# Performance work log

Measured on AMD Instinct MI355X. Metric: run time of the kernel, lower is better.

Reference implementation:

```python
import jax, jax.numpy as jnp
import numpy as np
from jax import lax

TEMPERATURE = 30.0
BN_EPS = 1e-5


def setup_inputs() -> dict:
    key = jax.random.key(0)
    ks = jax.random.split(key, 9)
    B, H, W, C_in = 32, 64, 64, 128
    n_filters, r_filters, n_kernels = 128, 4, 4
    x = jax.random.normal(ks[0], (B, H, W, C_in), dtype=jnp.float32)
    reduction_kernel = jax.random.normal(ks[1], (C_in, r_filters), dtype=jnp.float32) * 0.02
    attention_kernel = jax.random.normal(ks[2], (r_filters, n_kernels), dtype=jnp.float32) * 0.02
    conv_kernels = jax.random.normal(ks[3], (n_kernels, 3, 3, C_in, n_filters), dtype=jnp.float32) * 0.05
    bias = jax.random.normal(ks[4], (n_kernels, n_filters), dtype=jnp.float32) * 0.05
    bn_scale = jax.random.uniform(ks[5], (n_filters,), dtype=jnp.float32, minval=0.5, maxval=1.5)
    bn_bias = jax.random.normal(ks[6], (n_filters,), dtype=jnp.float32) * 0.1
    bn_mean = jax.random.normal(ks[7], (n_filters,), dtype=jnp.float32) * 0.1
    bn_var = jax.random.uniform(ks[8], (n_filters,), dtype=jnp.float32, minval=0.5, maxval=1.5)
    return {"x": x, "reduction_kernel": reduction_kernel, "attention_kernel": attention_kernel,
            "conv_kernels": conv_kernels, "bias": bias, "bn_scale": bn_scale, "bn_bias": bn_bias,
            "bn_mean": bn_mean, "bn_var": bn_var}


def reference(x, reduction_kernel, attention_kernel, conv_kernels, bias, bn_scale, bn_bias, bn_mean, bn_var):
    # x: [B,H,W,C_in] NHWC. Inference mode (training=False): BN uses running stats.
    B = x.shape[0]
    # Squeeze-style routing: global average pool -> reduce -> relu -> attention over experts.
    pool = jnp.mean(x, axis=(1, 2))                             # [B, C_in]
    pool_red = jax.nn.relu(pool @ reduction_kernel)             # [B, r]
    attention = jax.nn.softmax((pool_red @ attention_kernel) / TEMPERATURE, axis=-1)  # [B, K]
    # Soft mixture of conv expert kernels, per sample.
    w_mixed = jnp.einsum('bk,khwio->bhwio', attention, conv_kernels)  # [B,kH,kW,C_in,F]

    def per_sample_conv(xi, wi):
        # xi: [H,W,C_in], wi: [kH,kW,C_in,F]
        return lax.conv_general_dilated(xi[None], wi, window_strides=(1, 1), padding='SAME',
                                        dimension_numbers=('NHWC', 'HWIO', 'NHWC'))[0]

    y = jax.vmap(per_sample_conv)(x, w_mixed)                   # [B,H,W,F]
    b_mixed = attention @ bias                                  # [B, F]
    y = y + b_mixed[:, None, None, :]
    # BatchNorm (inference) + relu
    inv = bn_scale * lax.rsqrt(bn_var + BN_EPS)
    y = (y - bn_mean) * inv + bn_bias
    return jax.nn.relu(y)
```

## Files before the change

kernel.cpp:

```cpp
#include <hip/hip_runtime.h>

typedef short bf16x8 __attribute__((ext_vector_type(8)));
typedef float f32x4 __attribute__((ext_vector_type(4)));
typedef unsigned int u32x4 __attribute__((ext_vector_type(4)));
typedef unsigned short u16x4 __attribute__((ext_vector_type(4)));

__device__ __forceinline__ unsigned short f2bf(float f) {
  unsigned u = __builtin_bit_cast(unsigned, f);
  u = (u + 0x7FFFu + ((u >> 16) & 1u)) >> 16;
  return (unsigned short)u;
}

__global__ __launch_bounds__(256) void k_pool_cvt(const float* __restrict__ x,
                                                  unsigned short* __restrict__ xb,
                                                  float* __restrict__ pp) {
  const int slice = blockIdx.x;
  const int b = blockIdx.y;
  const int t = threadIdx.x;
  const int c4 = (t & 31) * 4;
  const int seg = t >> 5;
  const size_t base = ((size_t)b * 4096 + slice * 256 + seg * 32) * 128;
  const float* xp = x + base;
  unsigned short* xbp = xb + base;
  f32x4 s = {0.f, 0.f, 0.f, 0.f};
  for (int p = 0; p < 32; ++p) {
    f32x4 v = *(const f32x4*)(xp + p * 128 + c4);
    s += v;
    u16x4 h;
    h.x = f2bf(v.x); h.y = f2bf(v.y); h.z = f2bf(v.z); h.w = f2bf(v.w);
    *(u16x4*)(xbp + p * 128 + c4) = h;
  }
  __shared__ f32x4 red[256];
  red[t] = s;
  __syncthreads();
  if (t < 32) {
    f32x4 tot = red[t];
#pragma unroll
    for (int g = 1; g < 8; ++g) tot += red[g * 32 + t];
    *(f32x4*)(pp + (size_t)(b * 16 + slice) * 128 + t * 4) = tot;
  }
}

__global__ __launch_bounds__(128) void k_route(const float* __restrict__ pp,
    const float* __restrict__ redk, const float* __restrict__ attk,
    const float* __restrict__ bias, const float* __restrict__ bns,
    const float* __restrict__ bnb, const float* __restrict__ bnm,
    const float* __restrict__ bnv,
    float* __restrict__ att_ws, float* __restrict__ beta_ws,
    float* __restrict__ alpha_ws) {
  const int b = blockIdx.x, t = threadIdx.x;
  __shared__ float pool[128];
  __shared__ float att[4];
  {
    float s = 0.f;
    for (int i = 0; i < 16; ++i) s += pp[(size_t)(b * 16 + i) * 128 + t];
    pool[t] = s * (1.f / 4096.f);
  }
  __syncthreads();
  if (t == 0) {
    float pr[4];
    for (int r = 0; r < 4; ++r) {
      float s = 0.f;
      for (int c = 0; c < 128; ++c) s += pool[c] * redk[c * 4 + r];
      pr[r] = fmaxf(s, 0.f);
    }
    float lgt[4]; float mx = -1e30f;
    for (int k = 0; k < 4; ++k) {
      float s = 0.f;
      for (int r = 0; r < 4; ++r) s += pr[r] * attk[r * 4 + k];
      lgt[k] = s * (1.f / 30.f);
      mx = fmaxf(mx, lgt[k]);
    }
    float den = 0.f;
    for (int k = 0; k < 4; ++k) { lgt[k] = expf(lgt[k] - mx); den += lgt[k]; }
    for (int k = 0; k < 4; ++k) { att[k] = lgt[k] / den; att_ws[b * 4 + k] = att[k]; }
  }
  __syncthreads();
  {
    float bm = 0.f;
    for (int k = 0; k < 4; ++k) bm += att[k] * bias[k * 128 + t];
    const float inv = bns[t] * rsqrtf(bnv[t] + 1e-5f);
    beta_ws[b * 128 + t] = (bm - bnm[t]) * inv + bnb[t];
    alpha_ws[t] = inv;
  }
}

__global__ __launch_bounds__(256) void k_mixw(const float* __restrict__ ck,
                                              const float* __restrict__ att_ws,
                                              unsigned short* __restrict__ w_ws) {
  const int tap = blockIdx.x;
  const int b = blockIdx.y;
  const int t = threadIdx.x;
  const float a0 = att_ws[b * 4 + 0], a1 = att_ws[b * 4 + 1];
  const float a2 = att_ws[b * 4 + 2], a3 = att_ws[b * 4 + 3];
  const float* ckp = ck + (size_t)tap * 16384;
  __shared__ unsigned short lds_t[128 * 136];
#pragma unroll 4
  for (int it = 0; it < 16; ++it) {
    const int i4 = t + it * 256;
    const int idx = i4 * 4;
    const int c = idx >> 7, f = idx & 127;
    f32x4 v0 = *(const f32x4*)(ckp + idx);
    f32x4 v1 = *(const f32x4*)(ckp + idx + 147456);
    f32x4 v2 = *(const f32x4*)(ckp + idx + 2 * 147456);
    f32x4 v3 = *(const f32x4*)(ckp + idx + 3 * 147456);
#pragma unroll
    for (int e = 0; e < 4; ++e)
      lds_t[(f + e) * 136 + c] = f2bf(a0 * v0[e] + a1 * v1[e] + a2 * v2[e] + a3 * v3[e]);
  }
  __syncthreads();
#pragma unroll
  for (int it = 0; it < 8; ++it) {
    const int m = t + it * 256;
    const int f = m >> 4, oo = m & 15;
    const int h = oo >> 3, o = oo & 7;
    unsigned short* dst = w_ws + ((size_t)b * 18 + h * 9 + tap) * 8192
                        + (size_t)(f * 8 + (o ^ (f & 7))) * 8;
    *(bf16x8*)dst = *(const bf16x8*)(lds_t + f * 136 + oo * 8);
  }
}

__device__ __forceinline__ void stage_w16(char* dst, const unsigned short* src, int t) {
#pragma unroll
  for (int j = 0; j < 4; ++j) {
    const int i = t + j * 256;
    __builtin_amdgcn_global_load_lds(
        (const __attribute__((address_space(1))) void*)(src + (size_t)i * 8),
        (__attribute__((address_space(3))) void*)(dst + i * 16), 16, 0, 0);
  }
}

__device__ __forceinline__ void stage_x_half(char* xt, const unsigned short* xbp,
                                             int r0, int h, int t) {
#pragma unroll
  for (int j = 0; j < 12; ++j) {
    const int i = t + j * 256;
    const int jr = i >> 9;
    const int pix = (i & 511) >> 3;
    const int oct = i & 7;
    const int soct = oct ^ (pix & 7);
    const int rr = r0 - 1 + jr;
    char* dst = xt + i * 16;
    if ((unsigned)rr < 64u) {
      __builtin_amdgcn_global_load_lds(
          (const __attribute__((address_space(1))) void*)
              (xbp + ((size_t)(rr * 64 + pix)) * 128 + h * 64 + soct * 8),
          (__attribute__((address_space(3))) void*)dst, 16, 0, 0);
    } else {
      *(u32x4*)dst = (u32x4){0, 0, 0, 0};
    }
  }
}

__global__ __launch_bounds__(256, 2) void k_conv(const unsigned short* __restrict__ xb,
                                                 const unsigned short* __restrict__ w_ws,
                                                 const float* __restrict__ alpha_ws,
                                                 const float* __restrict__ beta_ws,
                                                 float* __restrict__ out) {
  extern __shared__ char lds[];
  char* xt = lds;
  char* wlds = lds + 49152;

  const int orig = blockIdx.x;
  const int wg = (orig & 7) * 64 + (orig >> 3);
  const int b = wg >> 4;
  const int tile = wg & 15;
  const int t = threadIdx.x;
  const int lane = t & 63, wm = t >> 6;
  const int lr = lane & 15, lg = lane >> 4;
  const int r0 = tile * 4;

  const unsigned short* xbp = xb + (size_t)b * 4096 * 128;
  const unsigned short* wsrc = w_ws + (size_t)b * 18 * 8192;

  f32x4 acc[4][8] = {};
  const bf16x8 zero = {};

  int abase[3][4];
  bool aval[3][4];
#pragma unroll
  for (int d = 0; d < 3; ++d)
#pragma unroll
    for (int mf = 0; mf < 4; ++mf) {
      const int col = mf * 16 + lr + d - 1;
      const bool v = (unsigned)col < 64u;
      aval[d][mf] = v;
      abase[d][mf] = v ? ((col * 128 + lg * 16) ^ ((col & 7) << 4)) : 0;
    }
  int bbase[8];
#pragma unroll
  for (int nf = 0; nf < 8; ++nf) {
    const int f = nf * 16 + lr;
    bbase[nf] = (f * 128 + lg * 16) ^ ((f & 7) << 4);
  }

  stage_x_half(xt, xbp, r0, 0, t);
  stage_w16(wlds, wsrc, t);
  asm volatile("s_waitcnt vmcnt(0) lgkmcnt(0)" ::: "memory");
  __builtin_amdgcn_s_barrier();
  asm volatile("" ::: "memory");

#pragma unroll
  for (int s = 0; s < 18; ++s) {
    const int tap = s % 9;
    char* cb = wlds + ((s & 1) << 14);
    if (s == 9) stage_x_half(xt, xbp, r0, 1, t);
    if (s < 17) stage_w16(wlds + (((s + 1) & 1) << 14),
                          wsrc + (size_t)(s + 1) * 8192, t);
    if (s == 9)       asm volatile("s_waitcnt vmcnt(4) lgkmcnt(0)" ::: "memory");
    else if (s < 17)  asm volatile("s_waitcnt vmcnt(4)" ::: "memory");
    else              asm volatile("s_waitcnt vmcnt(0)" ::: "memory");
    __builtin_amdgcn_s_barrier();
    asm volatile("" ::: "memory");

    const int d = tap % 3;
    const int jrow = wm + tap / 3;
#pragma unroll
    for (int kc = 0; kc < 2; ++kc) {
      const int kx = kc << 6;
      bf16x8 afr[4], bfr[8];
#pragma unroll
      for (int mf = 0; mf < 4; ++mf) {
        bf16x8 v = *(const bf16x8*)(xt + ((abase[d][mf] ^ kx) + jrow * 8192));
        afr[mf] = aval[d][mf] ? v : zero;
      }
#pragma unroll
      for (int nf = 0; nf < 8; ++nf)
        bfr[nf] = *(const bf16x8*)(cb + (bbase[nf] ^ kx));
      __builtin_amdgcn_s_setprio(1);
#pragma unroll
      for (int mf = 0; mf < 4; ++mf)
#pragma unroll
        for (int nf = 0; nf < 8; ++nf)
          acc[mf][nf] = __builtin_amdgcn_mfma_f32_16x16x32_bf16(afr[mf], bfr[nf],
                                                                acc[mf][nf], 0, 0, 0);
      __builtin_amdgcn_s_setprio(0);
    }
    asm volatile("" ::: "memory");
    __builtin_amdgcn_s_barrier();
  }

  float af[8], bt[8];
#pragma unroll
  for (int nf = 0; nf < 8; ++nf) {
    const int f = nf * 16 + lr;
    af[nf] = alpha_ws[f];
    bt[nf] = beta_ws[b * 128 + f];
  }
  float* op = out + (size_t)b * 4096 * 128;
  const int row = r0 + wm;
#pragma unroll
  for (int mf = 0; mf < 4; ++mf) {
#pragma unroll
    for (int r = 0; r < 4; ++r) {
      const int col = mf * 16 + lg * 4 + r;
#pragma unroll
      for (int nf = 0; nf < 8; ++nf) {
        const int f = nf * 16 + lr;
        const float v = acc[mf][nf][r] * af[nf] + bt[nf];
        op[(size_t)(row * 64 + col) * 128 + f] = fmaxf(v, 0.f);
      }
    }
  }
}

extern "C" void kernel_launch(void* const* d_in, const int* in_sizes, int n_in,
                              void* d_out, int out_size, void* d_ws, size_t ws_size,
                              hipStream_t stream) {
  const float* x    = (const float*)d_in[0];
  const float* redk = (const float*)d_in[1];
  const float* attk = (const float*)d_in[2];
  const float* ck   = (const float*)d_in[3];
  const float* bias = (const float*)d_in[4];
  const float* bns  = (const float*)d_in[5];
  const float* bnbb = (const float*)d_in[6];
  const float* bnm  = (const float*)d_in[7];
  const float* bnv  = (const float*)d_in[8];
  float* out = (float*)d_out;

  char* ws = (char*)d_ws;
  unsigned short* xb   = (unsigned short*)ws;
  unsigned short* w_ws = (unsigned short*)(ws + 33554432);
  float* pp       = (float*)(ws + 42991616);
  float* att_ws   = (float*)(ws + 43253760);
  float* beta_ws  = (float*)(ws + 43254272);
  float* alpha_ws = (float*)(ws + 43270656);

  k_pool_cvt<<<dim3(16, 32), 256, 0, stream>>>(x, xb, pp);
  k_route<<<32, 128, 0, stream>>>(pp, redk, attk, bias, bns, bnbb, bnm, bnv,
                                  att_ws, beta_ws, alpha_ws);
  k_mixw<<<dim3(9, 32), 256, 0, stream>>>(ck, att_ws, w_ws);
  k_conv<<<512, 256, 81920, stream>>>(xb, w_ws, alpha_ws, beta_ws, out);
}
```

Before: 89.35 us.

## Double conv row tile per workgroup and restructure mixed-weight kernel across batches

The conv kernel now computes 8 output rows per workgroup instead of 4. Each wave handles two rows, so every weight fragment loaded from LDS feeds twice as many MFMAs, and the grid halves to 256 blocks with larger LDS and one block per CU. The weight-mixing kernel is reorganised so each block loads one tap/channel/filter sub-tile of the expert kernels once and writes mixed bf16 weights for all 32 samples. This avoids re-reading the expert kernels for every sample. The cost is fewer resident waves per CU, more accumulator registers, and a non-unrolled stage loop that computes column offsets at run time.

```diff
diff --git a/kernel.cpp b/kernel.cpp
--- a/kernel.cpp
+++ b/kernel.cpp
@@ -88,35 +88,47 @@
 __global__ __launch_bounds__(256) void k_mixw(const float* __restrict__ ck,
                                               const float* __restrict__ att_ws,
                                               unsigned short* __restrict__ w_ws) {
-  const int tap = blockIdx.x;
-  const int b = blockIdx.y;
+  const int bx = blockIdx.x;
+  const int tap = bx >> 4;
+  const int cq = (bx >> 2) & 3;
+  const int fq = bx & 3;
   const int t = threadIdx.x;
-  const float a0 = att_ws[b * 4 + 0], a1 = att_ws[b * 4 + 1];
-  const float a2 = att_ws[b * 4 + 2], a3 = att_ws[b * 4 + 3];
-  const float* ckp = ck + (size_t)tap * 16384;
-  __shared__ unsigned short lds_t[128 * 136];
-#pragma unroll 4
-  for (int it = 0; it < 16; ++it) {
-    const int i4 = t + it * 256;
-    const int idx = i4 * 4;
-    const int c = idx >> 7, f = idx & 127;
-    f32x4 v0 = *(const f32x4*)(ckp + idx);
-    f32x4 v1 = *(const f32x4*)(ckp + idx + 147456);
-    f32x4 v2 = *(const f32x4*)(ckp + idx + 2 * 147456);
-    f32x4 v3 = *(const f32x4*)(ckp + idx + 3 * 147456);
-#pragma unroll
-    for (int e = 0; e < 4; ++e)
-      lds_t[(f + e) * 136 + c] = f2bf(a0 * v0[e] + a1 * v1[e] + a2 * v2[e] + a3 * v3[e]);
+  __shared__ float cw[4][32][32];
+  __shared__ float attl[128];
+  if (t < 128) attl[t] = att_ws[t];
+  {
+    const int k = t >> 6, c = (t & 63) >> 1, f0 = (t & 1) * 16;
+    const float* src = ck + ((size_t)(k * 9 + tap) * 128 + cq * 32 + c) * 128
+                          + fq * 32 + f0;
+    *(f32x4*)&cw[k][c][f0]      = *(const f32x4*)(src);
+    *(f32x4*)&cw[k][c][f0 + 4]  = *(const f32x4*)(src + 4);
+    *(f32x4*)&cw[k][c][f0 + 8]  = *(const f32x4*)(src + 8);
+    *(f32x4*)&cw[k][c][f0 + 12] = *(const f32x4*)(src + 12);
   }
   __syncthreads();
-#pragma unroll
-  for (int it = 0; it < 8; ++it) {
-    const int m = t + it * 256;
-    const int f = m >> 4, oo = m & 15;
-    const int h = oo >> 3, o = oo & 7;
-    unsigned short* dst = w_ws + ((size_t)b * 18 + h * 9 + tap) * 8192
-                        + (size_t)(f * 8 + (o ^ (f & 7))) * 8;
-    *(bf16x8*)dst = *(const bf16x8*)(lds_t + f * 136 + oo * 8);
+  const int f = t & 31, o = (t >> 5) & 3, sh = t >> 7;
+  const int fp = fq * 32 + f;
+  const int h = cq >> 1;
+  const int oslab = (cq & 1) * 4 + o;
+  const int chunk = fp * 8 + (oslab ^ (fp & 7));
+  float wv[4][8];
+#pragma unroll
+  for (int k = 0; k < 4; ++k)
+#pragma unroll
+    for (int j = 0; j < 8; ++j) wv[k][j] = cw[k][o * 8 + j][f];
+#pragma unroll
+  for (int bs = 0; bs < 16; ++bs) {
+    const int b = sh * 16 + bs;
+    const float a0 = attl[b * 4 + 0], a1 = attl[b * 4 + 1];
+    const float a2 = attl[b * 4 + 2], a3 = attl[b * 4 + 3];
+    bf16x8 ov;
+#pragma unroll
+    for (int j = 0; j < 8; ++j) {
+      const float v = a0 * wv[0][j] + a1 * wv[1][j] + a2 * wv[2][j] + a3 * wv[3][j];
+      ov[j] = (short)f2bf(v);
+    }
+    *(bf16x8*)(w_ws + (size_t)b * 147456 + (size_t)(h * 9 + tap) * 8192
+               + (size_t)chunk * 8) = ov;
   }
 }
 
@@ -133,7 +145,7 @@
 __device__ __forceinline__ void stage_x_half(char* xt, const unsigned short* xbp,
                                              int r0, int h, int t) {
 #pragma unroll
-  for (int j = 0; j < 12; ++j) {
+  for (int j = 0; j < 20; ++j) {
     const int i = t + j * 256;
     const int jr = i >> 9;
     const int pix = (i & 511) >> 3;
@@ -152,41 +164,30 @@
   }
 }
 
-__global__ __launch_bounds__(256, 2) void k_conv(const unsigned short* __restrict__ xb,
+__global__ __launch_bounds__(256, 1) void k_conv(const unsigned short* __restrict__ xb,
                                                  const unsigned short* __restrict__ w_ws,
                                                  const float* __restrict__ alpha_ws,
                                                  const float* __restrict__ beta_ws,
                                                  float* __restrict__ out) {
   extern __shared__ char lds[];
   char* xt = lds;
-  char* wlds = lds + 49152;
+  char* wlds = lds + 81920;
 
   const int orig = blockIdx.x;
-  const int wg = (orig & 7) * 64 + (orig >> 3);
-  const int b = wg >> 4;
-  const int tile = wg & 15;
+  const int wg = (orig & 7) * 32 + (orig >> 3);
+  const int b = wg >> 3;
+  const int tile = wg & 7;
   const int t = threadIdx.x;
   const int lane = t & 63, wm = t >> 6;
   const int lr = lane & 15, lg = lane >> 4;
-  const int r0 = tile * 4;
+  const int r0 = tile * 8;
 
   const unsigned short* xbp = xb + (size_t)b * 4096 * 128;
   const unsigned short* wsrc = w_ws + (size_t)b * 18 * 8192;
 
-  f32x4 acc[4][8] = {};
+  f32x4 acc[8][8] = {};
   const bf16x8 zero = {};
 
-  int abase[3][4];
-  bool aval[3][4];
-#pragma unroll
-  for (int d = 0; d < 3; ++d)
-#pragma unroll
-    for (int mf = 0; mf < 4; ++mf) {
-      const int col = mf * 16 + lr + d - 1;
-      const bool v = (unsigned)col < 64u;
-      aval[d][mf] = v;
-      abase[d][mf] = v ? ((col * 128 + lg * 16) ^ ((col & 7) << 4)) : 0;
-    }
   int bbase[8];
 #pragma unroll
   for (int nf = 0; nf < 8; ++nf) {
@@ -200,9 +201,10 @@
   __builtin_amdgcn_s_barrier();
   asm volatile("" ::: "memory");
 
-#pragma unroll
   for (int s = 0; s < 18; ++s) {
-    const int tap = s % 9;
+    const int tap = (s >= 9) ? s - 9 : s;
+    const int dr = (tap * 11) >> 5;
+    const int dw = tap - dr * 3;
     char* cb = wlds + ((s & 1) << 14);
     if (s == 9) stage_x_half(xt, xbp, r0, 1, t);
     if (s < 17) stage_w16(wlds + (((s + 1) & 1) << 14),
@@ -213,27 +215,39 @@
     __builtin_amdgcn_s_barrier();
     asm volatile("" ::: "memory");
 
-    const int d = tap % 3;
-    const int jrow = wm + tap / 3;
+    int cA[4]; bool vA[4];
+#pragma unroll
+    for (int cf = 0; cf < 4; ++cf) {
+      const int col = cf * 16 + lr + dw - 1;
+      vA[cf] = (unsigned)col < 64u;
+      const int cc = col & 63;
+      cA[cf] = (cc * 128 + lg * 16) ^ ((cc & 7) << 4);
+    }
+    const int ro0 = (2 * wm + dr) * 8192;
+
 #pragma unroll
     for (int kc = 0; kc < 2; ++kc) {
       const int kx = kc << 6;
-      bf16x8 afr[4], bfr[8];
-#pragma unroll
-      for (int mf = 0; mf < 4; ++mf) {
-        bf16x8 v = *(const bf16x8*)(xt + ((abase[d][mf] ^ kx) + jrow * 8192));
-        afr[mf] = aval[d][mf] ? v : zero;
-      }
+      bf16x8 afr[2][4], bfr[8];
+#pragma unroll
+      for (int rh = 0; rh < 2; ++rh)
+#pragma unroll
+        for (int cf = 0; cf < 4; ++cf) {
+          bf16x8 v = *(const bf16x8*)(xt + (ro0 + rh * 8192 + (cA[cf] ^ kx)));
+          afr[rh][cf] = vA[cf] ? v : zero;
+        }
 #pragma unroll
       for (int nf = 0; nf < 8; ++nf)
         bfr[nf] = *(const bf16x8*)(cb + (bbase[nf] ^ kx));
       __builtin_amdgcn_s_setprio(1);
 #pragma unroll
-      for (int mf = 0; mf < 4; ++mf)
-#pragma unroll
-        for (int nf = 0; nf < 8; ++nf)
-          acc[mf][nf] = __builtin_amdgcn_mfma_f32_16x16x32_bf16(afr[mf], bfr[nf],
-                                                                acc[mf][nf], 0, 0, 0);
+      for (int rh = 0; rh < 2; ++rh)
+#pragma unroll
+        for (int cf = 0; cf < 4; ++cf)
+#pragma unroll
+          for (int nf = 0; nf < 8; ++nf)
+            acc[rh * 4 + cf][nf] = __builtin_amdgcn_mfma_f32_16x16x32_bf16(
+                afr[rh][cf], bfr[nf], acc[rh * 4 + cf][nf], 0, 0, 0);
       __builtin_amdgcn_s_setprio(0);
     }
     asm volatile("" ::: "memory");
@@ -248,12 +262,12 @@
     bt[nf] = beta_ws[b * 128 + f];
   }
   float* op = out + (size_t)b * 4096 * 128;
-  const int row = r0 + wm;
-#pragma unroll
-  for (int mf = 0; mf < 4; ++mf) {
+#pragma unroll
+  for (int mf = 0; mf < 8; ++mf) {
+    const int row = r0 + 2 * wm + (mf >> 2);
 #pragma unroll
     for (int r = 0; r < 4; ++r) {
-      const int col = mf * 16 + lg * 4 + r;
+      const int col = (mf & 3) * 16 + lg * 4 + r;
 #pragma unroll
       for (int nf = 0; nf < 8; ++nf) {
         const int f = nf * 16 + lr;
@@ -286,9 +300,12 @@
   float* beta_ws  = (float*)(ws + 43254272);
   float* alpha_ws = (float*)(ws + 43270656);
 
+  (void)hipFuncSetAttribute((const void*)k_conv,
+                            hipFuncAttributeMaxDynamicSharedMemorySize, 114688);
+
   k_pool_cvt<<<dim3(16, 32), 256, 0, stream>>>(x, xb, pp);
   k_route<<<32, 128, 0, stream>>>(pp, redk, attk, bias, bns, bnbb, bnm, bnv,
                                   att_ws, beta_ws, alpha_ws);
-  k_mixw<<<dim3(9, 32), 256, 0, stream>>>(ck, att_ws, w_ws);
-  k_conv<<<512, 256, 81920, stream>>>(xb, w_ws, alpha_ws, beta_ws, out);
-}
+  k_mixw<<<144, 256, 0, stream>>>(ck, att_ws, w_ws);
+  k_conv<<<256, 256, 114688, stream>>>(xb, w_ws, alpha_ws, beta_ws, out);
+}
```

Measured after the change: 80.94 us. 9.4% less time.
